# Optimization experiments

Measured on AMD Instinct MI355X. Metric: run time of the kernel, lower is better.

## Reference

```python
import jax, jax.numpy as jnp
import numpy as np

# MLA decode with weight absorption + fp8-quantized absorbed weights + top-k sparse attention
H, R, NOPE, ROPE, V, HID = 32, 512, 128, 64, 128, 4096
B, S, TOPK = 64, 4096, 2048
SCALE = (NOPE + ROPE) ** -0.5  # qk_head_dim = 192
FP8_MAX = 448.0  # float8_e4m3fn finfo max


def _quant_fp8(w):
    """dynamic_per_batched_tensor_quant: per-tensor amax scale, e4m3 cast."""
    amax = jnp.maximum(jnp.max(jnp.abs(w)), 1e-10)
    s = FP8_MAX / amax
    wq = jnp.clip(w * s, -FP8_MAX, FP8_MAX).astype(jnp.float8_e4m3fn).astype(jnp.float32)
    return wq, (1.0 / s).astype(jnp.float32)


def _apply_rope(q_pe, positions):
    # neox-style rotary on the rope slice of q; k_pe in cache is pre-rotated
    half = ROPE // 2
    inv_freq = 1.0 / (10000.0 ** (jnp.arange(0, ROPE, 2, dtype=jnp.float32) / ROPE))
    freqs = positions.astype(jnp.float32)[:, None] * inv_freq        # [B, half]
    cos = jnp.cos(freqs)[:, None, :]                                  # [B,1,half]
    sin = jnp.sin(freqs)[:, None, :]
    q1, q2 = q_pe[..., :half], q_pe[..., half:]
    return jnp.concatenate([q1 * cos - q2 * sin, q2 * cos + q1 * sin], axis=-1)


def setup_inputs() -> dict:
    key = jax.random.key(0)
    ks = jax.random.split(key, 8)
    x = jax.random.normal(ks[0], (B, HID), dtype=jnp.float32)
    Wq = jax.random.normal(ks[1], (HID, H * (NOPE + ROPE)), dtype=jnp.float32) * 0.02
    W_UK = jax.random.normal(ks[2], (R, H, NOPE), dtype=jnp.float32) * 0.02
    W_UV = jax.random.normal(ks[3], (R, H, V), dtype=jnp.float32) * 0.02
    # weight absorption layouts from process_weights_after_loading
    W_K_raw = jnp.transpose(W_UK, (1, 0, 2))   # [H, R, NOPE]
    W_V_raw = jnp.transpose(W_UV, (1, 2, 0))   # [H, V, R]
    W_K, W_K_scale = _quant_fp8(W_K_raw)
    W_V, W_V_scale = _quant_fp8(W_V_raw)
    Wo = jax.random.normal(ks[4], (H * V, HID), dtype=jnp.float32) * 0.02
    kv_cache = jax.random.normal(ks[5], (B, S, R + ROPE), dtype=jnp.float32)
    topk_indices = jax.random.randint(ks[6], (B, TOPK), 0, S, dtype=jnp.int32)
    positions = jax.random.randint(ks[7], (B,), 0, S, dtype=jnp.int32)
    return {"x": x, "Wq": Wq, "W_K": W_K, "W_K_scale": W_K_scale,
            "W_V": W_V, "W_V_scale": W_V_scale, "Wo": Wo,
            "kv_cache": kv_cache, "topk_indices": topk_indices,
            "positions": positions}


def reference(x, Wq, W_K, W_K_scale, W_V, W_V_scale, Wo, kv_cache,
              topk_indices, positions):
    Bq = x.shape[0]
    # q projection + split (q_proj then split into nope/pe)
    q = (x @ Wq).reshape(Bq, H, NOPE + ROPE)
    q_nope, q_pe = q[..., :NOPE], q[..., NOPE:]
    # k up-projection absorption: fp8 bmm + dequant scale -> latent-space queries
    ql = jnp.einsum('bhn,hrn->bhr', q_nope, W_K) * W_K_scale   # [B,H,R]
    q_pe = _apply_rope(q_pe, positions)                         # [B,H,ROPE]
    # top-k sparse gather of latent KV cache
    kv_sel = jnp.take_along_axis(kv_cache, topk_indices[:, :, None], axis=1)  # [B,TOPK,R+ROPE]
    c_kv, k_pe = kv_sel[..., :R], kv_sel[..., R:]
    # absorbed MQA attention in latent space (single shared KV head)
    scores = (jnp.einsum('bhr,bkr->bhk', ql, c_kv)
              + jnp.einsum('bhd,bkd->bhk', q_pe, k_pe)) * SCALE  # [B,H,TOPK]
    attn = jax.nn.softmax(scores, axis=-1)
    o = jnp.einsum('bhk,bkr->bhr', attn, c_kv)                   # [B,H,R]
    # v up-projection (fp8 bmm + dequant) then o_proj
    out = jnp.einsum('bhr,hvr->bhv', o, W_V) * W_V_scale          # [B,H,V]
    return out.reshape(Bq, H * V) @ Wo                            # [B,HID]
```

## Files before the change

kernel.cpp:

```cpp
#include <hip/hip_runtime.h>
#include <hip/hip_bf16.h>
#include <math.h>

#define H_ 32
#define R_ 512
#define NOPE_ 128
#define ROPE_ 64
#define V_ 128
#define HID_ 4096
#define B_ 64
#define S_ 4096
#define TOPK_ 2048
#define DQ_ 192
#define NQ_ 6144
#define DKV_ 576
#define KCH_ 16
#define ACH_ 8
#define CHUNK_ 256
#define TILE_ 16
#define NG_ (CHUNK_/TILE_)
#define DGSTR_ 264
#define KRSZ_ (36*DGSTR_)
#define VTS_ 24

typedef __attribute__((ext_vector_type(8))) short bf16x8;
typedef __attribute__((ext_vector_type(4))) short s16x4;
typedef __attribute__((ext_vector_type(4))) float f32x4;
typedef __attribute__((ext_vector_type(16))) float f32x16;

__device__ __forceinline__ float4 ld4(const float* p) { return *reinterpret_cast<const float4*>(p); }
__device__ __forceinline__ short f2b(float f) {
  __hip_bfloat16 h = __float2bfloat16(f);
  short s; __builtin_memcpy(&s, &h, 2); return s;
}
__device__ __forceinline__ float b2f(short s) {
  union { unsigned u; float f; } x; x.u = ((unsigned)(unsigned short)s) << 16; return x.f;
}
__device__ __forceinline__ void split2(float v, short& h, short& l) {
  short hh = f2b(v);
  h = hh; l = f2b(v - b2f(hh));
}
__device__ __forceinline__ s16x4 tr_read(unsigned byte_addr) {
  s16x4 r;
  asm volatile("ds_read_b64_tr_b16 %0, %1" : "=v"(r) : "v"(byte_addr));
  return r;
}

__global__ __launch_bounds__(256) void gemm64_mfma(const float* __restrict__ A,
    const float* __restrict__ A2,
    const float* __restrict__ Bm, float* __restrict__ Cp, int N, int K) {
  __shared__ __align__(16) short Ah[64*40], Al[64*40];
  __shared__ __align__(16) short Bh[128*40], Bl[128*40];
  const int t = threadIdx.x;
  const int nt = blockIdx.x, kc = blockIdx.y;
  const int n0 = nt*128;
  const int kchunk = K / gridDim.y, kbeg = kc*kchunk;
  const int lane = t & 63, wid = t >> 6;
  const int lk = lane & 15, lg = lane >> 4;
  const int wm2 = wid >> 1, wn2 = wid & 1;
  const int kq = t & 7, ng = t >> 3;
  f32x4 acc[2][4];
  #pragma unroll
  for (int mi=0;mi<2;mi++)
    #pragma unroll
    for (int nj=0;nj<4;nj++) acc[mi][nj] = (f32x4){0.f,0.f,0.f,0.f};

  for (int k0 = kbeg; k0 < kbeg + kchunk; k0 += 32) {
    #pragma unroll
    for (int l=0;l<2;l++) {
      int idx = t + l*256;
      int m = idx >> 3, kq2 = idx & 7;
      float4 v = ld4(&A[(size_t)m*K + k0 + kq2*4]);
      if (A2) {
        float4 w = ld4(&A2[(size_t)m*K + k0 + kq2*4]);
        v.x+=w.x; v.y+=w.y; v.z+=w.z; v.w+=w.w;
      }
      short4 h4, l4;
      split2(v.x, h4.x, l4.x); split2(v.y, h4.y, l4.y);
      split2(v.z, h4.z, l4.z); split2(v.w, h4.w, l4.w);
      *reinterpret_cast<short4*>(&Ah[m*40 + kq2*4]) = h4;
      *reinterpret_cast<short4*>(&Al[m*40 + kq2*4]) = l4;
    }
    {
      float4 v0 = ld4(&Bm[(size_t)(k0+kq*4+0)*N + n0 + ng*4]);
      float4 v1 = ld4(&Bm[(size_t)(k0+kq*4+1)*N + n0 + ng*4]);
      float4 v2 = ld4(&Bm[(size_t)(k0+kq*4+2)*N + n0 + ng*4]);
      float4 v3 = ld4(&Bm[(size_t)(k0+kq*4+3)*N + n0 + ng*4]);
      short4 hj, lj;
      split2(v0.x,hj.x,lj.x); split2(v1.x,hj.y,lj.y); split2(v2.x,hj.z,lj.z); split2(v3.x,hj.w,lj.w);
      *reinterpret_cast<short4*>(&Bh[(ng*4+0)*40 + kq*4]) = hj;
      *reinterpret_cast<short4*>(&Bl[(ng*4+0)*40 + kq*4]) = lj;
      split2(v0.y,hj.x,lj.x); split2(v1.y,hj.y,lj.y); split2(v2.y,hj.z,lj.z); split2(v3.y,hj.w,lj.w);
      *reinterpret_cast<short4*>(&Bh[(ng*4+1)*40 + kq*4]) = hj;
      *reinterpret_cast<short4*>(&Bl[(ng*4+1)*40 + kq*4]) = lj;
      split2(v0.z,hj.x,lj.x); split2(v1.z,hj.y,lj.y); split2(v2.z,hj.z,lj.z); split2(v3.z,hj.w,lj.w);
      *reinterpret_cast<short4*>(&Bh[(ng*4+2)*40 + kq*4]) = hj;
      *reinterpret_cast<short4*>(&Bl[(ng*4+2)*40 + kq*4]) = lj;
      split2(v0.w,hj.x,lj.x); split2(v1.w,hj.y,lj.y); split2(v2.w,hj.z,lj.z); split2(v3.w,hj.w,lj.w);
      *reinterpret_cast<short4*>(&Bh[(ng*4+3)*40 + kq*4]) = hj;
      *reinterpret_cast<short4*>(&Bl[(ng*4+3)*40 + kq*4]) = lj;
    }
    __syncthreads();
    bf16x8 ah[2], al[2], bh[4], bl[4];
    #pragma unroll
    for (int mi=0;mi<2;mi++) {
      ah[mi] = *reinterpret_cast<const bf16x8*>(&Ah[(wm2*32+mi*16+lk)*40 + lg*8]);
      al[mi] = *reinterpret_cast<const bf16x8*>(&Al[(wm2*32+mi*16+lk)*40 + lg*8]);
    }
    #pragma unroll
    for (int nj=0;nj<4;nj++) {
      bh[nj] = *reinterpret_cast<const bf16x8*>(&Bh[(wn2*64+nj*16+lk)*40 + lg*8]);
      bl[nj] = *reinterpret_cast<const bf16x8*>(&Bl[(wn2*64+nj*16+lk)*40 + lg*8]);
    }
    #pragma unroll
    for (int mi=0;mi<2;mi++)
      #pragma unroll
      for (int nj=0;nj<4;nj++) {
        acc[mi][nj] = __builtin_amdgcn_mfma_f32_16x16x32_bf16(ah[mi], bh[nj], acc[mi][nj], 0, 0, 0);
        acc[mi][nj] = __builtin_amdgcn_mfma_f32_16x16x32_bf16(ah[mi], bl[nj], acc[mi][nj], 0, 0, 0);
        acc[mi][nj] = __builtin_amdgcn_mfma_f32_16x16x32_bf16(al[mi], bh[nj], acc[mi][nj], 0, 0, 0);
      }
    __syncthreads();
  }
  #pragma unroll
  for (int mi=0;mi<2;mi++)
    #pragma unroll
    for (int nj=0;nj<4;nj++)
      #pragma unroll
      for (int r=0;r<4;r++)
        Cp[((size_t)kc*64 + wm2*32 + mi*16 + lg*4 + r)*N + n0 + wn2*64 + nj*16 + lk] = acc[mi][nj][r];
}

__global__ __launch_bounds__(256) void gemm64x64_mfma(const float* __restrict__ A, int lda,
    const float* __restrict__ Bw, int ldb, int Bhstride,
    const float* __restrict__ scl, float smul,
    float* __restrict__ out, int ostride, int ohstride, int okcstride, int nk128) {
  __shared__ __align__(16) short Ah[64*136], Al[64*136], Bh[64*136];
  const int t = threadIdx.x;
  const int h = blockIdx.x, ct = blockIdx.y, kcz = blockIdx.z;
  const int koffs = kcz*nk128*128;
  const int lane = t & 63, wid = t >> 6;
  const int lk = lane & 15, lg = lane >> 4;
  const int wm2 = wid >> 1, wn2 = wid & 1;
  const int H = gridDim.x;
  f32x4 acc[2][2];
  #pragma unroll
  for (int mi=0;mi<2;mi++)
    #pragma unroll
    for (int nj=0;nj<2;nj++) acc[mi][nj] = (f32x4){0.f,0.f,0.f,0.f};

  for (int c=0; c<nk128; ++c) {
    if (c) __syncthreads();
    const int k0 = koffs + c*128;
    #pragma unroll
    for (int l=0;l<8;l++) {
      int idx = t + l*256;
      int m = idx >> 5, kq = idx & 31;
      float4 v = ld4(&A[((size_t)m*H + h)*lda + k0 + kq*4]);
      short4 h4, l4;
      split2(v.x,h4.x,l4.x); split2(v.y,h4.y,l4.y);
      split2(v.z,h4.z,l4.z); split2(v.w,h4.w,l4.w);
      *reinterpret_cast<short4*>(&Ah[m*136 + kq*4]) = h4;
      *reinterpret_cast<short4*>(&Al[m*136 + kq*4]) = l4;
      float4 w = ld4(&Bw[(size_t)h*Bhstride + (size_t)(ct*64 + m)*ldb + k0 + kq*4]);
      short4 b4; b4.x=f2b(w.x); b4.y=f2b(w.y); b4.z=f2b(w.z); b4.w=f2b(w.w);
      *reinterpret_cast<short4*>(&Bh[m*136 + kq*4]) = b4;
    }
    __syncthreads();
    #pragma unroll
    for (int ks=0; ks<4; ++ks) {
      bf16x8 ah[2], al[2], bh[2];
      #pragma unroll
      for (int mi=0;mi<2;mi++) {
        ah[mi] = *reinterpret_cast<const bf16x8*>(&Ah[(wm2*32+mi*16+lk)*136 + ks*32 + lg*8]);
        al[mi] = *reinterpret_cast<const bf16x8*>(&Al[(wm2*32+mi*16+lk)*136 + ks*32 + lg*8]);
      }
      #pragma unroll
      for (int nj=0;nj<2;nj++)
        bh[nj] = *reinterpret_cast<const bf16x8*>(&Bh[(wn2*32+nj*16+lk)*136 + ks*32 + lg*8]);
      #pragma unroll
      for (int mi=0;mi<2;mi++)
        #pragma unroll
        for (int nj=0;nj<2;nj++) {
          acc[mi][nj] = __builtin_amdgcn_mfma_f32_16x16x32_bf16(ah[mi], bh[nj], acc[mi][nj], 0, 0, 0);
          acc[mi][nj] = __builtin_amdgcn_mfma_f32_16x16x32_bf16(al[mi], bh[nj], acc[mi][nj], 0, 0, 0);
        }
    }
  }
  const float sc = scl[0]*smul;
  #pragma unroll
  for (int mi=0;mi<2;mi++)
    #pragma unroll
    for (int nj=0;nj<2;nj++)
      #pragma unroll
      for (int r=0;r<4;r++) {
        int row = wm2*32 + mi*16 + lg*4 + r;
        int col = ct*64 + wn2*32 + nj*16 + lk;
        out[(size_t)kcz*okcstride + (size_t)row*ostride + (size_t)h*ohstride + col] = acc[mi][nj][r]*sc;
      }
}

__global__ __launch_bounds__(256) void reduce_rope(const float* __restrict__ qp,
    const int* __restrict__ positions, float* __restrict__ qn, float* __restrict__ qfull) {
  __shared__ float pe[H_*ROPE_];
  const int b = blockIdx.x, t = threadIdx.x;
  for (int n = t*4; n < NQ_; n += 1024) {
    float4 s = make_float4(0.f,0.f,0.f,0.f);
    for (int c=0;c<KCH_;c++) {
      float4 v = ld4(&qp[((size_t)c*64 + b)*NQ_ + n]);
      s.x+=v.x; s.y+=v.y; s.z+=v.z; s.w+=v.w;
    }
    float vs[4] = {s.x,s.y,s.z,s.w};
    #pragma unroll
    for (int e=0;e<4;e++) {
      int nn = n+e; int h = nn/DQ_; int d = nn - h*DQ_;
      if (d < NOPE_) qn[((size_t)b*H_ + h)*NOPE_ + d] = vs[e];
      else pe[h*ROPE_ + (d-NOPE_)] = vs[e];
    }
  }
  __syncthreads();
  const float pos = (float)positions[b];
  const float SC = 0.0721687836487032f;
  for (int it = t; it < H_*32; it += 256) {
    int h = it >> 5, i = it & 31;
    float invf = (float)exp(-(double)i * 0.28782313662425574);
    float fr = pos * invf;
    float cs = cosf(fr), sn = sinf(fr);
    float q1 = pe[h*ROPE_ + i], q2 = pe[h*ROPE_ + 32 + i];
    qfull[((size_t)b*H_ + h)*DKV_ + R_ + i]      = (q1*cs - q2*sn)*SC;
    qfull[((size_t)b*H_ + h)*DKV_ + R_ + 32 + i] = (q2*cs + q1*sn)*SC;
  }
}

__global__ __launch_bounds__(256) void attn_chunk(const float* __restrict__ qfull,
    const float* __restrict__ kv, const int* __restrict__ topk,
    float* __restrict__ om, float* __restrict__ ol, float* __restrict__ op) {
  __shared__ __align__(16) short krows[2][KRSZ_];
  __shared__ __align__(16) short P_lds[H_*VTS_];
  __shared__ float Spart[2*16*33];
  __shared__ float fl[H_];
  __shared__ int tk_lds[CHUNK_];
  const int lin = blockIdx.x + 8*blockIdx.y;
  const int xcd = lin & 7, ixc = lin >> 3;
  const int b  = xcd*8 + (ixc & 7);
  const int kc = ixc >> 3;
  const int t = threadIdx.x;
  const int lane = t & 63, wid = t >> 6;
  const int wm = wid >> 1, dn = wid & 1;
  const int lk = lane & 15, lg = lane >> 4;
  const int l31 = lane & 31, hi = lane >> 5;
  const int h16 = wm*16 + lk;

  bf16x8 qf[9];
  {
    const float* qb = &qfull[((size_t)b*H_ + h16)*DKV_ + dn*288 + lg*8];
    #pragma unroll
    for (int ks=0; ks<9; ++ks) {
      float4 u = ld4(qb + ks*32);
      float4 v = ld4(qb + ks*32 + 4);
      bf16x8 f;
      f[0]=f2b(u.x); f[1]=f2b(u.y); f[2]=f2b(u.z); f[3]=f2b(u.w);
      f[4]=f2b(v.x); f[5]=f2b(v.y); f[6]=f2b(v.z); f[7]=f2b(v.w);
      qf[ks] = f;
    }
  }

  int row_l[9], coff_l[9], woff_l[9];
  #pragma unroll
  for (int l=0;l<9;l++) {
    int idx = t + l*256;
    int row = idx/144, c = idx - row*144;
    int d0 = c*4;
    row_l[l] = row; coff_l[l] = d0;
    woff_l[l] = (d0>>4)*DGSTR_ + row*16 + (d0&15);
  }
  const float* kvb = kv + (size_t)b*S_*DKV_;
  const int kbase = b*TOPK_ + kc*CHUNK_;
  tk_lds[t] = topk[kbase + t];
  __syncthreads();

  float4 stA[9], stB[9];
  #define ISSUE(ST, G) { \
    _Pragma("unroll") \
    for (int l=0;l<9;l++) { \
      int ki = tk_lds[(G)*TILE_ + row_l[l]]; \
      ST[l] = ld4(kvb + (size_t)ki*DKV_ + coff_l[l]); \
    } }
  #define WBUF(KB, ST) { \
    _Pragma("unroll") \
    for (int l=0;l<9;l++) { \
      short4 s4; s4.x=f2b(ST[l].x); s4.y=f2b(ST[l].y); s4.z=f2b(ST[l].z); s4.w=f2b(ST[l].w); \
      *reinterpret_cast<short4*>(&(KB)[woff_l[l]]) = s4; \
    } }

  ISSUE(stA, 0);
  WBUF(krows[0], stA);
  ISSUE(stA, 1);
  ISSUE(stB, 2);
  asm volatile("s_waitcnt lgkmcnt(0)\n\ts_barrier" ::: "memory");

  float m_run = -INFINITY, l_run = 0.f;
  f32x16 acc[4];
  #pragma unroll
  for (int tt=0;tt<4;tt++)
    #pragma unroll
    for (int i=0;i<16;i++) acc[tt][i] = 0.f;

  const int soff = (dn*18 + (lg>>1))*DGSTR_ + lk*16 + (lg&1)*8;
  const int i15 = lk;
  const unsigned trc = (unsigned)((((wid*8) + ((lane>>4)&1))*DGSTR_ + (hi*8 + (i15>>2))*16 + (i15&3)*4)*2);

  for (int g=0; g<NG_; ++g) {
    const int cur = g & 1;
    short* kb = krows[cur];
    f32x4 sacc = {0.f,0.f,0.f,0.f};
    #pragma unroll
    for (int ks=0; ks<9; ++ks) {
      bf16x8 af = *reinterpret_cast<const bf16x8*>(&kb[soff + ks*(2*DGSTR_)]);
      sacc = __builtin_amdgcn_mfma_f32_16x16x32_bf16(af, qf[ks], sacc, 0, 0, 0);
    }
    #pragma unroll
    for (int r=0;r<4;r++)
      Spart[dn*528 + (lg*4+r)*33 + h16] = sacc[r];
    asm volatile("s_waitcnt lgkmcnt(0)\n\ts_barrier" ::: "memory");

    float sfull[4];
    #pragma unroll
    for (int r=0;r<4;r++)
      sfull[r] = Spart[(lg*4+r)*33 + h16] + Spart[528 + (lg*4+r)*33 + h16];
    float tmax = fmaxf(fmaxf(sfull[0],sfull[1]), fmaxf(sfull[2],sfull[3]));
    tmax = fmaxf(tmax, __shfl_xor(tmax, 16));
    tmax = fmaxf(tmax, __shfl_xor(tmax, 32));
    float m_new = fmaxf(m_run, tmax);
    float fscale = __expf(m_run - m_new);
    m_run = m_new;
    float p0 = __expf(sfull[0]-m_new), p1 = __expf(sfull[1]-m_new);
    float p2 = __expf(sfull[2]-m_new), p3 = __expf(sfull[3]-m_new);
    float ps = (p0+p1)+(p2+p3);
    ps += __shfl_xor(ps, 16);
    ps += __shfl_xor(ps, 32);
    l_run = l_run*fscale + ps;
    if (dn==0) {
      short4 pk; pk.x=f2b(p0); pk.y=f2b(p1); pk.z=f2b(p2); pk.w=f2b(p3);
      *reinterpret_cast<short4*>(&P_lds[h16*VTS_ + lg*4]) = pk;
      if (lg==0) fl[h16] = fscale;
    }
    if ((g & 1) == 0) {
      if (g < NG_-1) WBUF(krows[cur^1], stA);
      if (g+3 < NG_) ISSUE(stA, g+3);
    } else {
      if (g < NG_-1) WBUF(krows[cur^1], stB);
      if (g+3 < NG_) ISSUE(stB, g+3);
    }
    asm volatile("s_waitcnt lgkmcnt(0)\n\ts_barrier" ::: "memory");

    float fsc = fl[l31];
    bf16x8 pf = *reinterpret_cast<const bf16x8*>(&P_lds[l31*VTS_ + hi*8]);
    unsigned kaddr = (unsigned)(unsigned long long)(void*)kb;
    s16x4 tr0_0 = tr_read(kaddr + trc + 0*1056);
    s16x4 tr1_0 = tr_read(kaddr + trc + 0*1056 + 128);
    s16x4 tr0_1 = tr_read(kaddr + trc + 1*1056);
    s16x4 tr1_1 = tr_read(kaddr + trc + 1*1056 + 128);
    s16x4 tr0_2 = tr_read(kaddr + trc + 2*1056);
    s16x4 tr1_2 = tr_read(kaddr + trc + 2*1056 + 128);
    s16x4 tr0_3 = tr_read(kaddr + trc + 3*1056);
    s16x4 tr1_3 = tr_read(kaddr + trc + 3*1056 + 128);
    #pragma unroll
    for (int tt=0;tt<4;tt++)
      #pragma unroll
      for (int i=0;i<16;i++) acc[tt][i] *= fsc;
    asm volatile("s_waitcnt lgkmcnt(0)" ::: "memory");
    __builtin_amdgcn_sched_barrier(0);
    {
      bf16x8 vf;
      vf[0]=tr0_0[0]; vf[1]=tr0_0[1]; vf[2]=tr0_0[2]; vf[3]=tr0_0[3];
      vf[4]=tr1_0[0]; vf[5]=tr1_0[1]; vf[6]=tr1_0[2]; vf[7]=tr1_0[3];
      acc[0] = __builtin_amdgcn_mfma_f32_32x32x16_bf16(vf, pf, acc[0], 0, 0, 0);
      vf[0]=tr0_1[0]; vf[1]=tr0_1[1]; vf[2]=tr0_1[2]; vf[3]=tr0_1[3];
      vf[4]=tr1_1[0]; vf[5]=tr1_1[1]; vf[6]=tr1_1[2]; vf[7]=tr1_1[3];
      acc[1] = __builtin_amdgcn_mfma_f32_32x32x16_bf16(vf, pf, acc[1], 0, 0, 0);
      vf[0]=tr0_2[0]; vf[1]=tr0_2[1]; vf[2]=tr0_2[2]; vf[3]=tr0_2[3];
      vf[4]=tr1_2[0]; vf[5]=tr1_2[1]; vf[6]=tr1_2[2]; vf[7]=tr1_2[3];
      acc[2] = __builtin_amdgcn_mfma_f32_32x32x16_bf16(vf, pf, acc[2], 0, 0, 0);
      vf[0]=tr0_3[0]; vf[1]=tr0_3[1]; vf[2]=tr0_3[2]; vf[3]=tr0_3[3];
      vf[4]=tr1_3[0]; vf[5]=tr1_3[1]; vf[6]=tr1_3[2]; vf[7]=tr1_3[3];
      acc[3] = __builtin_amdgcn_mfma_f32_32x32x16_bf16(vf, pf, acc[3], 0, 0, 0);
    }
  }

  if (dn==0 && lg==0) {
    om[(b*ACH_+kc)*H_ + h16] = m_run;
    ol[(b*ACH_+kc)*H_ + h16] = l_run;
  }
  #pragma unroll
  for (int tt=0;tt<4;tt++)
    #pragma unroll
    for (int q=0;q<4;q++) {
      float4 v = make_float4(acc[tt][4*q+0], acc[tt][4*q+1], acc[tt][4*q+2], acc[tt][4*q+3]);
      int r0 = wid*128 + tt*32 + 8*q + 4*hi;
      *reinterpret_cast<float4*>(&op[(((size_t)(b*ACH_+kc))*H_ + l31)*R_ + r0]) = v;
    }
  #undef ISSUE
  #undef WBUF
}

__global__ __launch_bounds__(128) void attn_merge(const float* __restrict__ om,
    const float* __restrict__ ol, const float* __restrict__ op, float* __restrict__ obuf) {
  const int bh = blockIdx.x;
  const int b = bh >> 5, h = bh & 31;
  const int t = threadIdx.x;
  float mv[8], lv[8], w[8];
  float M = -INFINITY;
  #pragma unroll
  for (int c=0;c<8;c++) { mv[c] = om[(b*ACH_+c)*H_ + h]; lv[c] = ol[(b*ACH_+c)*H_+h]; M = fmaxf(M, mv[c]); }
  float L = 0.f;
  #pragma unroll
  for (int c=0;c<8;c++) { w[c] = __expf(mv[c]-M); L += lv[c]*w[c]; }
  float inv = 1.0f / L;
  float4 s = make_float4(0.f,0.f,0.f,0.f);
  #pragma unroll
  for (int c=0;c<8;c++) {
    float4 v = ld4(&op[(((size_t)(b*ACH_+c))*H_ + h)*R_ + t*4]);
    s.x += v.x*w[c]; s.y += v.y*w[c]; s.z += v.z*w[c]; s.w += v.w*w[c];
  }
  s.x*=inv; s.y*=inv; s.z*=inv; s.w*=inv;
  *reinterpret_cast<float4*>(&obuf[((size_t)b*H_+h)*R_ + t*4]) = s;
}

__global__ __launch_bounds__(256) void reduce_out(const float* __restrict__ op2, float* __restrict__ out) {
  int idx = blockIdx.x*256 + threadIdx.x;
  float4 s = make_float4(0.f,0.f,0.f,0.f);
  #pragma unroll
  for (int c=0;c<KCH_;c++) {
    float4 v = ld4(&op2[(size_t)c*B_*HID_ + (size_t)idx*4]);
    s.x+=v.x; s.y+=v.y; s.z+=v.z; s.w+=v.w;
  }
  *reinterpret_cast<float4*>(&out[(size_t)idx*4]) = s;
}

extern "C" void kernel_launch(void* const* d_in, const int* in_sizes, int n_in,
                              void* d_out, int out_size, void* d_ws, size_t ws_size,
                              hipStream_t stream) {
  (void)in_sizes; (void)n_in; (void)out_size; (void)ws_size;
  const float* x   = (const float*)d_in[0];
  const float* Wq  = (const float*)d_in[1];
  const float* WK  = (const float*)d_in[2];
  const float* WKs = (const float*)d_in[3];
  const float* WV  = (const float*)d_in[4];
  const float* WVs = (const float*)d_in[5];
  const float* Wo  = (const float*)d_in[6];
  const float* kv  = (const float*)d_in[7];
  const int* topk  = (const int*)d_in[8];
  const int* pos   = (const int*)d_in[9];
  float* ws = (float*)d_ws;
  float* qp    = ws;
  float* qn    = qp    + (size_t)KCH_*64*6144;
  float* qfull = qn    + (size_t)64*32*128;
  float* om    = qfull + (size_t)64*32*576;
  float* ol    = om    + (size_t)64*8*32;
  float* op    = ol    + (size_t)64*8*32;
  float* obuf  = op    + (size_t)64*8*32*512;
  float* midp  = obuf  + (size_t)64*32*512;
  float* op2   = midp  + (size_t)2*64*4096;
  float* outf  = (float*)d_out;
  const float SC = 0.0721687836487032f;

  gemm64_mfma<<<dim3(48,KCH_),256,0,stream>>>(x, nullptr, Wq, qp, NQ_, HID_);
  reduce_rope<<<64,256,0,stream>>>(qp, pos, qn, qfull);
  gemm64x64_mfma<<<dim3(32,8,1),256,0,stream>>>(qn, NOPE_, WK, NOPE_, R_*NOPE_,
      WKs, SC, qfull, H_*DKV_, DKV_, 0, 1);
  attn_chunk<<<dim3(8,64),256,0,stream>>>(qfull, kv, topk, om, ol, op);
  attn_merge<<<2048,128,0,stream>>>(om, ol, op, obuf);
  gemm64x64_mfma<<<dim3(32,2,2),256,0,stream>>>(obuf, R_, WV, R_, V_*R_,
      WVs, 1.0f, midp, HID_, V_, B_*HID_, 2);
  gemm64_mfma<<<dim3(32,KCH_),256,0,stream>>>(midp, midp + (size_t)B_*HID_, Wo, op2, HID_, HID_);
  reduce_out<<<256,256,0,stream>>>(op2, outf);
}
```

Baseline: 187.6 us.

## Software-pipeline the PV MFMA block one tile behind the QK score MFMAs

Moves the P·V accumulation for tile g-1 into iteration g, right after the QK MFMAs for tile g, with a final PV block after the loop. Previously the PV block ran after the second barrier of each iteration. The aim is to let the PV LDS transpose reads and MFMAs overlap with the score MFMAs and softmax, cutting per-tile serialization between barriers. The previous KV buffer, P tile and scale values stay valid until the next barrier, but register pressure rises and correctness now depends on that buffer ordering.

```diff
diff --git a/kernel.cpp b/kernel.cpp
--- a/kernel.cpp
+++ b/kernel.cpp
@@ -310,15 +310,51 @@
   const int i15 = lk;
   const unsigned trc = (unsigned)((((wid*8) + ((lane>>4)&1))*DGSTR_ + (hi*8 + (i15>>2))*16 + (i15&3)*4)*2);
 
+  #define PVBLOCK(KBP) { \
+    float fsc = fl[l31]; \
+    bf16x8 pf = *reinterpret_cast<const bf16x8*>(&P_lds[l31*VTS_ + hi*8]); \
+    unsigned kaddr = (unsigned)(unsigned long long)(void*)(KBP); \
+    s16x4 tr0_0 = tr_read(kaddr + trc + 0*1056); \
+    s16x4 tr1_0 = tr_read(kaddr + trc + 0*1056 + 128); \
+    s16x4 tr0_1 = tr_read(kaddr + trc + 1*1056); \
+    s16x4 tr1_1 = tr_read(kaddr + trc + 1*1056 + 128); \
+    s16x4 tr0_2 = tr_read(kaddr + trc + 2*1056); \
+    s16x4 tr1_2 = tr_read(kaddr + trc + 2*1056 + 128); \
+    s16x4 tr0_3 = tr_read(kaddr + trc + 3*1056); \
+    s16x4 tr1_3 = tr_read(kaddr + trc + 3*1056 + 128); \
+    _Pragma("unroll") \
+    for (int tt=0;tt<4;tt++) \
+      _Pragma("unroll") \
+      for (int i=0;i<16;i++) acc[tt][i] *= fsc; \
+    asm volatile("s_waitcnt lgkmcnt(0)" ::: "memory"); \
+    __builtin_amdgcn_sched_barrier(0); \
+    bf16x8 vf; \
+    vf[0]=tr0_0[0]; vf[1]=tr0_0[1]; vf[2]=tr0_0[2]; vf[3]=tr0_0[3]; \
+    vf[4]=tr1_0[0]; vf[5]=tr1_0[1]; vf[6]=tr1_0[2]; vf[7]=tr1_0[3]; \
+    acc[0] = __builtin_amdgcn_mfma_f32_32x32x16_bf16(vf, pf, acc[0], 0, 0, 0); \
+    vf[0]=tr0_1[0]; vf[1]=tr0_1[1]; vf[2]=tr0_1[2]; vf[3]=tr0_1[3]; \
+    vf[4]=tr1_1[0]; vf[5]=tr1_1[1]; vf[6]=tr1_1[2]; vf[7]=tr1_1[3]; \
+    acc[1] = __builtin_amdgcn_mfma_f32_32x32x16_bf16(vf, pf, acc[1], 0, 0, 0); \
+    vf[0]=tr0_2[0]; vf[1]=tr0_2[1]; vf[2]=tr0_2[2]; vf[3]=tr0_2[3]; \
+    vf[4]=tr1_2[0]; vf[5]=tr1_2[1]; vf[6]=tr1_2[2]; vf[7]=tr1_2[3]; \
+    acc[2] = __builtin_amdgcn_mfma_f32_32x32x16_bf16(vf, pf, acc[2], 0, 0, 0); \
+    vf[0]=tr0_3[0]; vf[1]=tr0_3[1]; vf[2]=tr0_3[2]; vf[3]=tr0_3[3]; \
+    vf[4]=tr1_3[0]; vf[5]=tr1_3[1]; vf[6]=tr1_3[2]; vf[7]=tr1_3[3]; \
+    acc[3] = __builtin_amdgcn_mfma_f32_32x32x16_bf16(vf, pf, acc[3], 0, 0, 0); \
+  }
+
   for (int g=0; g<NG_; ++g) {
     const int cur = g & 1;
-    short* kb = krows[cur];
+    short* kb  = krows[cur];
+    short* kbp = krows[cur^1];
+
     f32x4 sacc = {0.f,0.f,0.f,0.f};
     #pragma unroll
     for (int ks=0; ks<9; ++ks) {
       bf16x8 af = *reinterpret_cast<const bf16x8*>(&kb[soff + ks*(2*DGSTR_)]);
       sacc = __builtin_amdgcn_mfma_f32_16x16x32_bf16(af, qf[ks], sacc, 0, 0, 0);
     }
+    if (g) PVBLOCK(kbp);
     #pragma unroll
     for (int r=0;r<4;r++)
       Spart[dn*528 + (lg*4+r)*33 + h16] = sacc[r];
@@ -353,40 +389,9 @@
       if (g+3 < NG_) ISSUE(stB, g+3);
     }
     asm volatile("s_waitcnt lgkmcnt(0)\n\ts_barrier" ::: "memory");
-
-    float fsc = fl[l31];
-    bf16x8 pf = *reinterpret_cast<const bf16x8*>(&P_lds[l31*VTS_ + hi*8]);
-    unsigned kaddr = (unsigned)(unsigned long long)(void*)kb;
-    s16x4 tr0_0 = tr_read(kaddr + trc + 0*1056);
-    s16x4 tr1_0 = tr_read(kaddr + trc + 0*1056 + 128);
-    s16x4 tr0_1 = tr_read(kaddr + trc + 1*1056);
-    s16x4 tr1_1 = tr_read(kaddr + trc + 1*1056 + 128);
-    s16x4 tr0_2 = tr_read(kaddr + trc + 2*1056);
-    s16x4 tr1_2 = tr_read(kaddr + trc + 2*1056 + 128);
-    s16x4 tr0_3 = tr_read(kaddr + trc + 3*1056);
-    s16x4 tr1_3 = tr_read(kaddr + trc + 3*1056 + 128);
-    #pragma unroll
-    for (int tt=0;tt<4;tt++)
-      #pragma unroll
-      for (int i=0;i<16;i++) acc[tt][i] *= fsc;
-    asm volatile("s_waitcnt lgkmcnt(0)" ::: "memory");
-    __builtin_amdgcn_sched_barrier(0);
-    {
-      bf16x8 vf;
-      vf[0]=tr0_0[0]; vf[1]=tr0_0[1]; vf[2]=tr0_0[2]; vf[3]=tr0_0[3];
-      vf[4]=tr1_0[0]; vf[5]=tr1_0[1]; vf[6]=tr1_0[2]; vf[7]=tr1_0[3];
-      acc[0] = __builtin_amdgcn_mfma_f32_32x32x16_bf16(vf, pf, acc[0], 0, 0, 0);
-      vf[0]=tr0_1[0]; vf[1]=tr0_1[1]; vf[2]=tr0_1[2]; vf[3]=tr0_1[3];
-      vf[4]=tr1_1[0]; vf[5]=tr1_1[1]; vf[6]=tr1_1[2]; vf[7]=tr1_1[3];
-      acc[1] = __builtin_amdgcn_mfma_f32_32x32x16_bf16(vf, pf, acc[1], 0, 0, 0);
-      vf[0]=tr0_2[0]; vf[1]=tr0_2[1]; vf[2]=tr0_2[2]; vf[3]=tr0_2[3];
-      vf[4]=tr1_2[0]; vf[5]=tr1_2[1]; vf[6]=tr1_2[2]; vf[7]=tr1_2[3];
-      acc[2] = __builtin_amdgcn_mfma_f32_32x32x16_bf16(vf, pf, acc[2], 0, 0, 0);
-      vf[0]=tr0_3[0]; vf[1]=tr0_3[1]; vf[2]=tr0_3[2]; vf[3]=tr0_3[3];
-      vf[4]=tr1_3[0]; vf[5]=tr1_3[1]; vf[6]=tr1_3[2]; vf[7]=tr1_3[3];
-      acc[3] = __builtin_amdgcn_mfma_f32_32x32x16_bf16(vf, pf, acc[3], 0, 0, 0);
-    }
-  }
+  }
+
+  PVBLOCK(krows[(NG_-1)&1]);
 
   if (dn==0 && lg==0) {
     om[(b*ACH_+kc)*H_ + h16] = m_run;
@@ -402,6 +407,7 @@
     }
   #undef ISSUE
   #undef WBUF
+  #undef PVBLOCK
 }
 
 __global__ __launch_bounds__(128) void attn_merge(const float* __restrict__ om,
```

Measured after the change: 179.3 us (median of 2 runs). 4.4% less time.
